# Kernel tuning notes

Measured on AMD Instinct MI355X. Metric: run time of the kernel, lower is better.

## Reference

```python
import jax, jax.numpy as jnp
import numpy as np

NUM_LAYERS = 2
D_MODEL = 64
D_INNER = 128   # expand * d_model
D_STATE = 128   # min(2*input_size, 256)
DT_RANK = 4     # ceil(d_model / 16)
D_CONV = 4
HIDDEN = 64


def _causal_dwconv(x, w, b):
    # x: [B, L, C], w: [C, K], b: [C]  -- causal depthwise conv (left pad K-1)
    K = w.shape[1]
    L = x.shape[1]
    xp = jnp.pad(x, ((0, 0), (K - 1, 0), (0, 0)))
    y = sum(xp[:, k:k + L, :] * w[:, k][None, None, :] for k in range(K))
    return y + b


def _selective_scan(u, delta, A, B, C, Dp):
    # u, delta: [b,L,d]; A: [d,n]; B, C: [b,L,n]; Dp: [d]
    dA = jnp.exp(jnp.einsum('bld,dn->lbdn', delta, A))          # [L,b,d,n]
    dBu = jnp.einsum('bld,bln,bld->lbdn', delta, B, u)           # [L,b,d,n]
    Ct = jnp.swapaxes(C, 0, 1)                                   # [L,b,n]

    def step(h, inp):
        dA_t, dBu_t, C_t = inp
        h = dA_t * h + dBu_t                                     # [b,d,n]
        y = jnp.einsum('bdn,bn->bd', h, C_t)
        return h, y

    h0 = jnp.zeros(dA.shape[1:], dA.dtype)
    _, ys = jax.lax.scan(step, h0, (dA, dBu, Ct))                # ys: [L,b,d]
    return jnp.swapaxes(ys, 0, 1) + u * Dp


def _mamba_layer(x, in_w, conv_w, conv_b, xproj_w, dt_w, dt_b, A_log, Dp, out_w):
    xz = x @ in_w.T                                              # [B,L,2*d_inner]
    xi, z = jnp.split(xz, 2, axis=-1)
    xi = jax.nn.silu(_causal_dwconv(xi, conv_w, conv_b))
    xdbl = xi @ xproj_w.T                                        # [B,L,dt_rank+2*d_state]
    delta = jax.nn.softplus(xdbl[..., :DT_RANK] @ dt_w.T + dt_b)
    Bm = xdbl[..., DT_RANK:DT_RANK + D_STATE]
    Cm = xdbl[..., DT_RANK + D_STATE:]
    A = -jnp.exp(A_log)
    y = _selective_scan(xi, delta, A, Bm, Cm, Dp)
    y = y * jax.nn.silu(z)
    return y @ out_w.T


def setup_inputs() -> dict:
    key = jax.random.key(0)
    ks = jax.random.split(key, 10)
    B, L = 4, 1024
    s = 0.05
    x = jax.random.normal(ks[0], (B, L, D_MODEL), dtype=jnp.float32)
    in_proj_w = jax.random.normal(ks[1], (NUM_LAYERS, 2 * D_INNER, D_MODEL)) * s
    conv_w = jax.random.normal(ks[2], (NUM_LAYERS, D_INNER, D_CONV)) * 0.2
    conv_b = jax.random.normal(ks[3], (NUM_LAYERS, D_INNER)) * 0.02
    x_proj_w = jax.random.normal(ks[4], (NUM_LAYERS, DT_RANK + 2 * D_STATE, D_INNER)) * s
    dt_w = jax.random.normal(ks[5], (NUM_LAYERS, D_INNER, DT_RANK)) * 0.1
    dt_b = jnp.full((NUM_LAYERS, D_INNER), -4.6, dtype=jnp.float32)  # softplus -> ~0.01
    # S4D-real init: A_log = log(1..d_state)
    A_log = jnp.log(jnp.broadcast_to(
        jnp.arange(1, D_STATE + 1, dtype=jnp.float32), (NUM_LAYERS, D_INNER, D_STATE)))
    D = jnp.ones((NUM_LAYERS, D_INNER), dtype=jnp.float32)
    out_proj_w = jax.random.normal(ks[6], (NUM_LAYERS, D_MODEL, D_INNER)) * s
    fc_w = jax.random.normal(ks[7], (HIDDEN, D_MODEL)) * s
    fc_b = jax.random.normal(ks[8], (HIDDEN,)) * 0.02
    return {"x": x, "in_proj_w": in_proj_w, "conv_w": conv_w, "conv_b": conv_b,
            "x_proj_w": x_proj_w, "dt_w": dt_w, "dt_b": dt_b, "A_log": A_log,
            "D": D, "out_proj_w": out_proj_w, "fc_w": fc_w, "fc_b": fc_b}


def reference(x, in_proj_w, conv_w, conv_b, x_proj_w, dt_w, dt_b, A_log, D, out_proj_w, fc_w, fc_b):
    h = x
    for l in range(NUM_LAYERS):
        h = _mamba_layer(h, in_proj_w[l], conv_w[l], conv_b[l], x_proj_w[l],
                         dt_w[l], dt_b[l], A_log[l], D[l], out_proj_w[l])
    return h @ fc_w.T + fc_b
```

## Files before the change

### kernel.cpp

```cpp
#include <hip/hip_runtime.h>
#include <hip/hip_bf16.h>

#define BB 4
#define LL 1024
#define DM 64
#define DI 128
#define DS 128
#define DTR 4
#define KC 4
#define RT 8
#define GRP 8
#define CS 64
#define NC 16
#define FQL 32
#define L2E 1.44269504f

#define XWT_OFF   0
#define INWT_OFF  65536
#define OWT_OFF   98304
#define CWT_OFF   114688
#define CB_OFF    115712
#define DTWT_OFF  115968
#define DTB_OFF   116992
#define XWDT_OFF  117248
#define WT_TOTAL  118272

__device__ __forceinline__ float silu_f(float x) { return x / (1.f + __expf(-x)); }
__device__ __forceinline__ float ex2(float x) { return __builtin_amdgcn_exp2f(x); }

__device__ __forceinline__ float ldf(const void* p, long i, unsigned bf) {
    return bf ? __bfloat162float(((const __hip_bfloat16*)p)[i]) : ((const float*)p)[i];
}

__device__ __forceinline__ void fma4(float4& acc, float s, const float4 w) {
    acc.x = fmaf(s, w.x, acc.x); acc.y = fmaf(s, w.y, acc.y);
    acc.z = fmaf(s, w.z, acc.z); acc.w = fmaf(s, w.w, acc.w);
}

__device__ __forceinline__ void probe_flags(const void* dtb, const void* fcw,
                                            unsigned& bfe, unsigned& bfw) {
    unsigned w = *(const unsigned*)dtb;
    bfe = (w == 0xC093C093u) ? 1u : 0u;
    const unsigned* p = (const unsigned*)fcw;
    int cnt = 0;
    for (int i = 0; i < 32; ++i) {
        unsigned m = p[i] & 0x7FFFu;
        if (m >= 0x3000u && m < 0x4200u) cnt++;
    }
    bfw = (cnt >= 28) ? 1u : 0u;
}

__global__ __launch_bounds__(256) void k_prep(
        const void* __restrict__ inw, const void* __restrict__ xw,
        const void* __restrict__ ow, const void* __restrict__ cw,
        const void* __restrict__ cb, const void* __restrict__ dtw,
        const void* __restrict__ dtb, const void* __restrict__ fcw,
        unsigned* __restrict__ flags, float* __restrict__ WT) {
    unsigned bfe, bfw;
    probe_flags(dtb, fcw, bfe, bfw);
    int bid = blockIdx.x, tid = threadIdx.x;
    if (bid < 28) {
        const void* src; long soff; int srcK; float* dst; int dstN; int n0, k0;
        if (bid < 16) {
            int l = bid >> 3, kt = (bid >> 2) & 1, nt = bid & 3;
            src = xw; srcK = 128; soff = (long)l * 260 * 128 + 4 * 128;
            n0 = nt * 64; k0 = kt * 64; dst = WT + XWT_OFF + l * 32768; dstN = 256;
        } else if (bid < 24) {
            int b2 = bid - 16, l = b2 >> 2, nt = b2 & 3;
            src = inw; srcK = 64; soff = (long)l * 256 * 64;
            n0 = nt * 64; k0 = 0; dst = WT + INWT_OFF + l * 16384; dstN = 256;
        } else {
            int b2 = bid - 24, l = b2 >> 1, kt = b2 & 1;
            src = ow; srcK = 128; soff = (long)l * 64 * 128;
            n0 = 0; k0 = kt * 64; dst = WT + OWT_OFF + l * 8192; dstN = 64;
        }
        __shared__ float tile[64 * 65];
        for (int i = tid; i < 4096; i += 256) {
            int ln = i >> 6, lk = i & 63;
            tile[ln * 65 + lk] = ldf(src, soff + (long)(n0 + ln) * srcK + k0 + lk, bfw);
        }
        __syncthreads();
        for (int i = tid; i < 4096; i += 256) {
            int lk = i >> 6, ln = i & 63;
            dst[(long)(k0 + lk) * dstN + n0 + ln] = tile[ln * 65 + lk];
        }
    } else {
        if (tid == 0) { flags[0] = bfe; flags[1] = bfw; flags[2] = bfe & bfw; }
        for (int j = tid; j < 1024; j += 256) {
            int l = j >> 9, t = (j >> 7) & 3, d = j & 127;
            WT[CWT_OFF + j] = ldf(cw, (long)l * 512 + d * 4 + t, bfw);
        }
        for (int j = tid; j < 256; j += 256) WT[CB_OFF + j] = ldf(cb, j, bfw);
        for (int j = tid; j < 1024; j += 256) {
            int l = j >> 9, r = (j >> 7) & 3, d = j & 127;
            WT[DTWT_OFF + j] = ldf(dtw, (long)l * 512 + d * 4 + r, bfw);
        }
        for (int j = tid; j < 256; j += 256) WT[DTB_OFF + j] = ldf(dtb, j, bfe);
        for (int j = tid; j < 1024; j += 256) {
            int l = j >> 9, rem = j & 511;
            WT[XWDT_OFF + j] = ldf(xw, (long)l * 260 * 128 + rem, bfw);
        }
    }
}

__global__ __launch_bounds__(256) void k_inx(
        const void* __restrict__ xin, int xin_probe,
        const float* __restrict__ inwT,
        const float* __restrict__ cwT, const float* __restrict__ cbF,
        const float* __restrict__ xwT, const float* __restrict__ xwdtF,
        const float* __restrict__ dtwT, const float* __restrict__ dtbF,
        const unsigned* __restrict__ flags,
        float* __restrict__ sz, float* __restrict__ xiw,
        float* __restrict__ dlt,
        float* __restrict__ Bm, float* __restrict__ Cm) {
    unsigned bfx = xin_probe ? flags[0] : 0u;
    int row0 = blockIdx.x * RT;
    int b = row0 >> 10, l0 = row0 & (LL - 1);
    int tid = threadIdx.x, lane = tid & 63, g = tid >> 6;
    __shared__ float xst[12 * DM];
    __shared__ float xc[12 * DI];
    __shared__ float act[RT * DI];
    __shared__ float dtp[RT * DTR];
    for (int i = tid; i < 12 * DM; i += 256) {
        int r = i >> 6;
        int l = l0 + r - (KC - 1);
        xst[i] = (l >= 0 && l < LL)
                 ? ldf(xin, ((long)b * LL + l) * DM + (i & 63), bfx) : 0.f;
    }
    __syncthreads();
    {
        const float4* wt4 = (const float4*)inwT;
        float4 acc[3];
        acc[0] = make_float4(0.f, 0.f, 0.f, 0.f);
        acc[1] = make_float4(0.f, 0.f, 0.f, 0.f);
        acc[2] = make_float4(0.f, 0.f, 0.f, 0.f);
#pragma unroll 4
        for (int k4 = 0; k4 < DM / 4; ++k4) {
            float4 w0 = wt4[(k4 * 4 + 0) * 64 + lane];
            float4 w1 = wt4[(k4 * 4 + 1) * 64 + lane];
            float4 w2 = wt4[(k4 * 4 + 2) * 64 + lane];
            float4 w3 = wt4[(k4 * 4 + 3) * 64 + lane];
#pragma unroll
            for (int r = 0; r < 3; ++r) {
                float4 av = *(const float4*)&xst[(g * 3 + r) * DM + k4 * 4];
                fma4(acc[r], av.x, w0); fma4(acc[r], av.y, w1);
                fma4(acc[r], av.z, w2); fma4(acc[r], av.w, w3);
            }
        }
        int n0 = lane * 4;
#pragma unroll
        for (int r = 0; r < 3; ++r) {
            int rr = g * 3 + r;
            if (n0 < DI) {
                *(float4*)&xc[rr * DI + n0] = acc[r];
            } else if (rr >= KC - 1 && rr < KC - 1 + RT) {
                float4 v;
                v.x = silu_f(acc[r].x); v.y = silu_f(acc[r].y);
                v.z = silu_f(acc[r].z); v.w = silu_f(acc[r].w);
                *(float4*)&sz[(size_t)(row0 + rr - (KC - 1)) * DI + (n0 - DI)] = v;
            }
        }
    }
    __syncthreads();
    for (int i = tid; i < RT * DI; i += 256) {
        int r = i >> 7, d = i & 127;
        float a = cbF[d];
#pragma unroll
        for (int t = 0; t < KC; ++t)
            a = fmaf(xc[(r + t) * DI + d], cwT[t * DI + d], a);
        float v = silu_f(a);
        act[i] = v;
        xiw[(size_t)(row0 + r) * DI + d] = v;
    }
    __syncthreads();
    {
        const float4* wt4 = (const float4*)xwT;
        float4 acc[2];
        acc[0] = make_float4(0.f, 0.f, 0.f, 0.f);
        acc[1] = make_float4(0.f, 0.f, 0.f, 0.f);
#pragma unroll 8
        for (int k4 = 0; k4 < DI / 4; ++k4) {
            float4 w0 = wt4[(k4 * 4 + 0) * 64 + lane];
            float4 w1 = wt4[(k4 * 4 + 1) * 64 + lane];
            float4 w2 = wt4[(k4 * 4 + 2) * 64 + lane];
            float4 w3 = wt4[(k4 * 4 + 3) * 64 + lane];
#pragma unroll
            for (int r = 0; r < 2; ++r) {
                float4 av = *(const float4*)&act[(g * 2 + r) * DI + k4 * 4];
                fma4(acc[r], av.x, w0); fma4(acc[r], av.y, w1);
                fma4(acc[r], av.z, w2); fma4(acc[r], av.w, w3);
            }
        }
        int n0 = lane * 4;
#pragma unroll
        for (int r = 0; r < 2; ++r) {
            int row = row0 + g * 2 + r;
            if (n0 < DS) *(float4*)&Bm[(size_t)row * DS + n0] = acc[r];
            else         *(float4*)&Cm[(size_t)row * DS + (n0 - DS)] = acc[r];
        }
    }
    if (tid < RT * DTR) {
        int r = tid >> 2, i = tid & 3;
        float a = 0.f;
#pragma unroll
        for (int k4 = 0; k4 < DI / 4; ++k4) {
            float4 av = *(const float4*)&act[r * DI + k4 * 4];
            float4 wv = *(const float4*)&xwdtF[i * DI + k4 * 4];
            a = fmaf(av.x, wv.x, a); a = fmaf(av.y, wv.y, a);
            a = fmaf(av.z, wv.z, a); a = fmaf(av.w, wv.w, a);
        }
        dtp[tid] = a;
    }
    __syncthreads();
    if (tid < DI) {
        float dw0 = dtwT[0 * DI + tid], dw1 = dtwT[1 * DI + tid];
        float dw2 = dtwT[2 * DI + tid], dw3 = dtwT[3 * DI + tid];
        float bv = dtbF[tid];
#pragma unroll
        for (int r = 0; r < RT; ++r) {
            float a = bv;
            a = fmaf(dtp[r * 4 + 0], dw0, a);
            a = fmaf(dtp[r * 4 + 1], dw1, a);
            a = fmaf(dtp[r * 4 + 2], dw2, a);
            a = fmaf(dtp[r * 4 + 3], dw3, a);
            dlt[(size_t)(row0 + r) * DI + tid] = (a > 20.f) ? a : log1pf(__expf(a));
        }
    }
}

__global__ __launch_bounds__(512) void k_scan1(
        const float* __restrict__ dlt, const float* __restrict__ xiw,
        const float* __restrict__ Bm, const float* __restrict__ Cm,
        const void* __restrict__ Alog, long aoff,
        const void* __restrict__ Dp, long doff,
        const unsigned* __restrict__ flags,
        float* __restrict__ hend, float* __restrict__ S,
        float* __restrict__ y) {
    __shared__ float Bsh[FQL][DS];
    __shared__ float Csh[FQL][DS];
    __shared__ float dsh[8][CS];
    __shared__ float dush[8][CS];
    __shared__ float ysh[CS][8];
    __shared__ float Wred[8 * 520];
    int gid = blockIdx.x;
    int dg = gid / (BB * NC);
    int bc = gid % (BB * NC);
    int b = bc / NC, c = bc % NC;
    int d0 = dg * 8;
    int tid = threadIdx.x, w = tid >> 6, t = tid & 63;
    int d = d0 + w, c0 = c * CS;
    unsigned bfe = flags[0];
    float A0 = -L2E * __expf(ldf(Alog, aoff + (long)d * DS + 2 * t, bfe));
    float A1 = -L2E * __expf(ldf(Alog, aoff + (long)d * DS + 2 * t + 1, bfe));
    {
        size_t src = ((size_t)b * LL + c0 + t) * DI + d0 + w;
        float dl = dlt[src], ul = xiw[src];
        dsh[w][t] = dl;
        dush[w][t] = dl * ul;
        ysh[t][w] = ul * ldf(Dp, doff + d0 + w, bfe);
    }
    float* Wl = Wred + w * 520;
    int rbase = (t >> 3) * 65 + (t & 7) * 8;
    float h0 = 0.f, h1v = 0.f, sumd = 0.f;
    for (int hh = 0; hh < 2; ++hh) {
        __syncthreads();
        for (int i = tid; i < FQL * 32; i += 512) {
            int r = i >> 5, c4 = (i & 31) * 4;
            size_t g = ((size_t)b * LL + c0 + hh * FQL + r) * DS + c4;
            *(float4*)&Bsh[r][c4] = *(const float4*)&Bm[g];
            *(float4*)&Csh[r][c4] = *(const float4*)&Cm[g];
        }
        __syncthreads();
        for (int li = 0; li < FQL; li += GRP) {
            int lg = hh * FQL + li;
            float dl[GRP], du[GRP], ea0[GRP], ea1[GRP], cv[GRP];
            float2 Bv[GRP], Cv[GRP];
#pragma unroll
            for (int s = 0; s < GRP; ++s) {
                dl[s] = dsh[w][lg + s];
                du[s] = dush[w][lg + s];
                Bv[s] = ((const float2*)Bsh[li + s])[t];
                Cv[s] = ((const float2*)Csh[li + s])[t];
            }
#pragma unroll
            for (int s = 0; s < GRP; ++s) {
                ea0[s] = ex2(dl[s] * A0);
                ea1[s] = ex2(dl[s] * A1);
                sumd += dl[s];
            }
#pragma unroll
            for (int s = 0; s < GRP; ++s) {
                h0  = fmaf(ea0[s], h0,  du[s] * Bv[s].x);
                h1v = fmaf(ea1[s], h1v, du[s] * Bv[s].y);
                cv[s] = fmaf(h0, Cv[s].x, h1v * Cv[s].y);
            }
#pragma unroll
            for (int s = 0; s < GRP; ++s) Wl[s * 65 + t] = cv[s];
            float pt = 0.f;
#pragma unroll
            for (int j = 0; j < 8; ++j) pt += Wl[rbase + j];
            pt += __shfl_xor(pt, 1, 64);
            pt += __shfl_xor(pt, 2, 64);
            pt += __shfl_xor(pt, 4, 64);
            if ((t & 7) == 0) ysh[lg + (t >> 3)][w] += pt;
        }
    }
    if (c < NC - 1) {
        size_t hbase = (((size_t)b * DI + d) * NC + c) * DS;
        ((float2*)(hend + hbase))[t] = make_float2(h0, h1v);
        if (t == 0) S[((size_t)b * DI + d) * NC + c] = sumd;
    }
    __syncthreads();
    for (int i = tid; i < CS * 8; i += 512) {
        int l = i >> 3, dd = i & 7;
        y[((size_t)b * LL + c0 + l) * DI + d0 + dd] = ysh[l][dd];
    }
}

__global__ __launch_bounds__(512) void k_scan2(
        const float* __restrict__ dlt, const float* __restrict__ Cm,
        const void* __restrict__ Alog, long aoff,
        const unsigned* __restrict__ flags,
        const float* __restrict__ hend, const float* __restrict__ S,
        float* __restrict__ y) {
    __shared__ float Csh[FQL][DS];
    __shared__ float cdsh[8][CS];
    __shared__ float ysh[CS][8];
    __shared__ float Wred[8 * 520];
    int gid = blockIdx.x;
    int dg = gid / (BB * (NC - 1));
    int bc = gid % (BB * (NC - 1));
    int b = bc / (NC - 1), c = bc % (NC - 1) + 1;
    int d0 = dg * 8;
    int tid = threadIdx.x, w = tid >> 6, t = tid & 63;
    int d = d0 + w, c0 = c * CS;
    unsigned bfe = flags[0];
    float A0 = -L2E * __expf(ldf(Alog, aoff + (long)d * DS + 2 * t, bfe));
    float A1 = -L2E * __expf(ldf(Alog, aoff + (long)d * DS + 2 * t + 1, bfe));
    {
        float a = dlt[((size_t)b * LL + c0 + t) * DI + d0 + w];
#pragma unroll
        for (int off = 1; off < 64; off <<= 1) {
            float nn = __shfl(a, t - off, 64);
            if (t >= off) a += nn;
        }
        cdsh[w][t] = a;
    }
    float hi0 = 0.f, hi1 = 0.f, ssum = 0.f;
    const float2* hep = (const float2*)(hend + (((size_t)b * DI + d) * NC) * DS);
    const float* Sp = S + ((size_t)b * DI + d) * NC;
    for (int cc = c - 1; cc >= 0; --cc) {
        float2 he = hep[(size_t)cc * (DS / 2) + t];
        hi0 = fmaf(ex2(A0 * ssum), he.x, hi0);
        hi1 = fmaf(ex2(A1 * ssum), he.y, hi1);
        ssum += Sp[cc];
    }
    float* Wl = Wred + w * 520;
    int rbase = (t >> 3) * 65 + (t & 7) * 8;
    for (int hh = 0; hh < 2; ++hh) {
        __syncthreads();
        for (int i = tid; i < FQL * 32; i += 512) {
            int r = i >> 5, c4 = (i & 31) * 4;
            *(float4*)&Csh[r][c4] =
                *(const float4*)&Cm[((size_t)b * LL + c0 + hh * FQL + r) * DS + c4];
        }
        __syncthreads();
        for (int li = 0; li < FQL; li += GRP) {
            int lg = hh * FQL + li;
            float cd[GRP], ea0[GRP], ea1[GRP], cv[GRP];
            float2 Cv[GRP];
#pragma unroll
            for (int s = 0; s < GRP; ++s) {
                cd[s] = cdsh[w][lg + s];
                Cv[s] = ((const float2*)Csh[li + s])[t];
            }
#pragma unroll
            for (int s = 0; s < GRP; ++s) {
                ea0[s] = ex2(cd[s] * A0);
                ea1[s] = ex2(cd[s] * A1);
            }
#pragma unroll
            for (int s = 0; s < GRP; ++s)
                cv[s] = fmaf(hi0 * ea0[s], Cv[s].x, hi1 * ea1[s] * Cv[s].y);
#pragma unroll
            for (int s = 0; s < GRP; ++s) Wl[s * 65 + t] = cv[s];
            float pt = 0.f;
#pragma unroll
            for (int j = 0; j < 8; ++j) pt += Wl[rbase + j];
            pt += __shfl_xor(pt, 1, 64);
            pt += __shfl_xor(pt, 2, 64);
            pt += __shfl_xor(pt, 4, 64);
            if ((t & 7) == 0) ysh[lg + (t >> 3)][w] = pt;
        }
    }
    __syncthreads();
    for (int i = tid; i < CS * 8; i += 512) {
        int l = i >> 3, dd = i & 7;
        size_t idx = ((size_t)b * LL + c0 + l) * DI + d0 + dd;
        y[idx] += ysh[l][dd];
    }
}

__global__ __launch_bounds__(256) void k_out(
        const float* __restrict__ y, const float* __restrict__ sz,
        const float* __restrict__ owT, float* __restrict__ hout) {
    int row0 = blockIdx.x * RT;
    int tid = threadIdx.x, n = tid & 63, g = tid >> 6;
    __shared__ float act[RT * DI];
    for (int i = tid; i < RT * DI; i += 256) {
        size_t idx = (size_t)(row0 + (i >> 7)) * DI + (i & 127);
        act[i] = y[idx] * sz[idx];
    }
    __syncthreads();
    float acc[2] = {0.f, 0.f};
#pragma unroll 8
    for (int k4 = 0; k4 < DI / 4; ++k4) {
        float w0 = owT[(k4 * 4 + 0) * DM + n];
        float w1 = owT[(k4 * 4 + 1) * DM + n];
        float w2 = owT[(k4 * 4 + 2) * DM + n];
        float w3 = owT[(k4 * 4 + 3) * DM + n];
#pragma unroll
        for (int r = 0; r < 2; ++r) {
            float4 av = *(const float4*)&act[(g * 2 + r) * DI + k4 * 4];
            acc[r] = fmaf(av.x, w0, acc[r]); acc[r] = fmaf(av.y, w1, acc[r]);
            acc[r] = fmaf(av.z, w2, acc[r]); acc[r] = fmaf(av.w, w3, acc[r]);
        }
    }
#pragma unroll
    for (int r = 0; r < 2; ++r)
        hout[(size_t)(row0 + g * 2 + r) * DM + n] = acc[r];
}

__global__ __launch_bounds__(256) void k_outfc(
        const float* __restrict__ y, const float* __restrict__ sz,
        const float* __restrict__ owT,
        const void* __restrict__ fw, const void* __restrict__ fb,
        const unsigned* __restrict__ flags, void* __restrict__ out) {
    unsigned bfw = flags[1], obf = flags[2];
    int row0 = blockIdx.x * RT;
    int tid = threadIdx.x, n = tid & 63, g = tid >> 6;
    __shared__ float act[RT * DI];
    __shared__ float wsh[DM * 65];
    __shared__ float hsh[RT * DM];
    for (int i = tid; i < RT * DI; i += 256) {
        size_t idx = (size_t)(row0 + (i >> 7)) * DI + (i & 127);
        act[i] = y[idx] * sz[idx];
    }
    for (int i = tid; i < DM * DM; i += 256) {
        int nn = i >> 6, k = i & 63;
        wsh[k * 65 + nn] = ldf(fw, i, bfw);
    }
    __syncthreads();
    float acc[2] = {0.f, 0.f};
#pragma unroll 8
    for (int k4 = 0; k4 < DI / 4; ++k4) {
        float w0 = owT[(k4 * 4 + 0) * DM + n];
        float w1 = owT[(k4 * 4 + 1) * DM + n];
        float w2 = owT[(k4 * 4 + 2) * DM + n];
        float w3 = owT[(k4 * 4 + 3) * DM + n];
#pragma unroll
        for (int r = 0; r < 2; ++r) {
            float4 av = *(const float4*)&act[(g * 2 + r) * DI + k4 * 4];
            acc[r] = fmaf(av.x, w0, acc[r]); acc[r] = fmaf(av.y, w1, acc[r]);
            acc[r] = fmaf(av.z, w2, acc[r]); acc[r] = fmaf(av.w, w3, acc[r]);
        }
    }
#pragma unroll
    for (int r = 0; r < 2; ++r) hsh[(g * 2 + r) * DM + n] = acc[r];
    __syncthreads();
    float bv = ldf(fb, n, bfw);
    float acc2[2] = {bv, bv};
#pragma unroll 8
    for (int k4 = 0; k4 < DM / 4; ++k4) {
        float w0 = wsh[(k4 * 4 + 0) * 65 + n];
        float w1 = wsh[(k4 * 4 + 1) * 65 + n];
        float w2 = wsh[(k4 * 4 + 2) * 65 + n];
        float w3 = wsh[(k4 * 4 + 3) * 65 + n];
#pragma unroll
        for (int r = 0; r < 2; ++r) {
            float4 av = *(const float4*)&hsh[(g * 2 + r) * DM + k4 * 4];
            acc2[r] = fmaf(av.x, w0, acc2[r]); acc2[r] = fmaf(av.y, w1, acc2[r]);
            acc2[r] = fmaf(av.z, w2, acc2[r]); acc2[r] = fmaf(av.w, w3, acc2[r]);
        }
    }
#pragma unroll
    for (int r = 0; r < 2; ++r) {
        size_t idx = (size_t)(row0 + g * 2 + r) * DM + n;
        if (obf) ((__hip_bfloat16*)out)[idx] = __float2bfloat16(acc2[r]);
        else     ((float*)out)[idx] = acc2[r];
    }
}

extern "C" void kernel_launch(void* const* d_in, const int* in_sizes, int n_in,
                              void* d_out, int out_size, void* d_ws, size_t ws_size,
                              hipStream_t stream) {
    const void* x    = d_in[0];
    const void* inw  = d_in[1];
    const void* cw   = d_in[2];
    const void* cb   = d_in[3];
    const void* xw   = d_in[4];
    const void* dtw  = d_in[5];
    const void* dtb  = d_in[6];
    const void* Alog = d_in[7];
    const void* Dp   = d_in[8];
    const void* ow   = d_in[9];
    const void* fcw  = d_in[10];
    const void* fcb  = d_in[11];

    const size_t NBL = (size_t)BB * LL;
    const int GB = (int)(NBL / RT);
    unsigned* flags = (unsigned*)d_ws;
    float* base = (float*)d_ws + 64;
    float* h1   = base;
    float* sz   = h1 + 262144;
    float* xiw  = sz + 524288;
    float* dlt  = xiw + 524288;
    float* Bmw  = dlt + 524288;
    float* Cmw  = Bmw + 524288;
    float* yw   = Cmw + 524288;
    float* hend = yw + 524288;
    float* S    = hend + 1048576;
    float* WT   = S + 8192;

    k_prep<<<29, 256, 0, stream>>>(inw, xw, ow, cw, cb, dtw, dtb, fcw, flags, WT);

    for (int l = 0; l < 2; ++l) {
        const void* xin = (l == 0) ? x : (const void*)h1;
        int xmode = (l == 0) ? 1 : 0;
        k_inx<<<GB, 256, 0, stream>>>(xin, xmode,
                                      WT + INWT_OFF + l * 16384,
                                      WT + CWT_OFF + l * 512, WT + CB_OFF + l * 128,
                                      WT + XWT_OFF + l * 32768, WT + XWDT_OFF + l * 512,
                                      WT + DTWT_OFF + l * 512, WT + DTB_OFF + l * 128,
                                      flags, sz, xiw, dlt, Bmw, Cmw);
        long ao = (long)l * DI * DS;
        long dof = (long)l * DI;
        k_scan1<<<16 * BB * NC, 512, 0, stream>>>(
            dlt, xiw, Bmw, Cmw, Alog, ao, Dp, dof, flags, hend, S, yw);
        k_scan2<<<16 * BB * (NC - 1), 512, 0, stream>>>(
            dlt, Cmw, Alog, ao, flags, hend, S, yw);
        if (l == 0) {
            k_out<<<GB, 256, 0, stream>>>(yw, sz, WT + OWT_OFF, h1);
        } else {
            k_outfc<<<GB, 256, 0, stream>>>(yw, sz, WT + OWT_OFF + 8192,
                                            fcw, fcb, flags, d_out);
        }
    }
}
```

Measured before the change: 291.7 us.

## Fuse two-pass chunked scan into one persistent kernel and fuse out/in projections

Merges the two chunked selective-scan kernels into one persistent kernel. Each chunk publishes its end state and delta sum with release flags, and later chunks spin-wait on those flags to fold in the carried state. It also fuses layer-0's output projection with layer-1's input projection, conv and x-projection, recomputing three halo rows per block. This cuts kernel launches and the y read-modify-write round trip, at the cost of cross-block spin waits that depend on all producer blocks being co-resident and on the ordering of work units.

```diff
diff --git a/kernel.cpp b/kernel.cpp
--- a/kernel.cpp
+++ b/kernel.cpp
@@ -13,6 +13,7 @@
 #define CS 64
 #define NC 16
 #define FQL 32
+#define NU 1024
 #define L2E 1.44269504f
 
 #define XWT_OFF   0
@@ -55,7 +56,8 @@
         const void* __restrict__ ow, const void* __restrict__ cw,
         const void* __restrict__ cb, const void* __restrict__ dtw,
         const void* __restrict__ dtb, const void* __restrict__ fcw,
-        unsigned* __restrict__ flags, float* __restrict__ WT) {
+        unsigned* __restrict__ flags, float* __restrict__ WT,
+        unsigned* __restrict__ FL) {
     unsigned bfe, bfw;
     probe_flags(dtb, fcw, bfe, bfw);
     int bid = blockIdx.x, tid = threadIdx.x;
@@ -86,6 +88,7 @@
         }
     } else {
         if (tid == 0) { flags[0] = bfe; flags[1] = bfw; flags[2] = bfe & bfw; }
+        for (int j = tid; j < 2 * NU; j += 256) FL[j] = 0u;
         for (int j = tid; j < 1024; j += 256) {
             int l = j >> 9, t = (j >> 7) & 3, d = j & 127;
             WT[CWT_OFF + j] = ldf(cw, (long)l * 512 + d * 4 + t, bfw);
@@ -228,207 +231,307 @@
     }
 }
 
-__global__ __launch_bounds__(512) void k_scan1(
+__global__ __launch_bounds__(512) void k_scanM(
         const float* __restrict__ dlt, const float* __restrict__ xiw,
         const float* __restrict__ Bm, const float* __restrict__ Cm,
         const void* __restrict__ Alog, long aoff,
         const void* __restrict__ Dp, long doff,
         const unsigned* __restrict__ flags,
-        float* __restrict__ hend, float* __restrict__ S,
+        unsigned long long* __restrict__ hend, float* __restrict__ S,
+        unsigned* __restrict__ FL, int lay,
         float* __restrict__ y) {
+    __shared__ float Csh[CS][DS];
     __shared__ float Bsh[FQL][DS];
-    __shared__ float Csh[FQL][DS];
     __shared__ float dsh[8][CS];
     __shared__ float dush[8][CS];
-    __shared__ float ysh[CS][8];
-    __shared__ float Wred[8 * 520];
-    int gid = blockIdx.x;
-    int dg = gid / (BB * NC);
-    int bc = gid % (BB * NC);
-    int b = bc / NC, c = bc % NC;
-    int d0 = dg * 8;
-    int tid = threadIdx.x, w = tid >> 6, t = tid & 63;
-    int d = d0 + w, c0 = c * CS;
-    unsigned bfe = flags[0];
-    float A0 = -L2E * __expf(ldf(Alog, aoff + (long)d * DS + 2 * t, bfe));
-    float A1 = -L2E * __expf(ldf(Alog, aoff + (long)d * DS + 2 * t + 1, bfe));
-    {
-        size_t src = ((size_t)b * LL + c0 + t) * DI + d0 + w;
-        float dl = dlt[src], ul = xiw[src];
-        dsh[w][t] = dl;
-        dush[w][t] = dl * ul;
-        ysh[t][w] = ul * ldf(Dp, doff + d0 + w, bfe);
-    }
-    float* Wl = Wred + w * 520;
-    int rbase = (t >> 3) * 65 + (t & 7) * 8;
-    float h0 = 0.f, h1v = 0.f, sumd = 0.f;
-    for (int hh = 0; hh < 2; ++hh) {
-        __syncthreads();
-        for (int i = tid; i < FQL * 32; i += 512) {
-            int r = i >> 5, c4 = (i & 31) * 4;
-            size_t g = ((size_t)b * LL + c0 + hh * FQL + r) * DS + c4;
-            *(float4*)&Bsh[r][c4] = *(const float4*)&Bm[g];
-            *(float4*)&Csh[r][c4] = *(const float4*)&Cm[g];
-        }
-        __syncthreads();
-        for (int li = 0; li < FQL; li += GRP) {
-            int lg = hh * FQL + li;
-            float dl[GRP], du[GRP], ea0[GRP], ea1[GRP], cv[GRP];
-            float2 Bv[GRP], Cv[GRP];
-#pragma unroll
-            for (int s = 0; s < GRP; ++s) {
-                dl[s] = dsh[w][lg + s];
-                du[s] = dush[w][lg + s];
-                Bv[s] = ((const float2*)Bsh[li + s])[t];
-                Cv[s] = ((const float2*)Csh[li + s])[t];
-            }
-#pragma unroll
-            for (int s = 0; s < GRP; ++s) {
-                ea0[s] = ex2(dl[s] * A0);
-                ea1[s] = ex2(dl[s] * A1);
-                sumd += dl[s];
-            }
-#pragma unroll
-            for (int s = 0; s < GRP; ++s) {
-                h0  = fmaf(ea0[s], h0,  du[s] * Bv[s].x);
-                h1v = fmaf(ea1[s], h1v, du[s] * Bv[s].y);
-                cv[s] = fmaf(h0, Cv[s].x, h1v * Cv[s].y);
-            }
-#pragma unroll
-            for (int s = 0; s < GRP; ++s) Wl[s * 65 + t] = cv[s];
-            float pt = 0.f;
-#pragma unroll
-            for (int j = 0; j < 8; ++j) pt += Wl[rbase + j];
-            pt += __shfl_xor(pt, 1, 64);
-            pt += __shfl_xor(pt, 2, 64);
-            pt += __shfl_xor(pt, 4, 64);
-            if ((t & 7) == 0) ysh[lg + (t >> 3)][w] += pt;
-        }
-    }
-    if (c < NC - 1) {
-        size_t hbase = (((size_t)b * DI + d) * NC + c) * DS;
-        ((float2*)(hend + hbase))[t] = make_float2(h0, h1v);
-        if (t == 0) S[((size_t)b * DI + d) * NC + c] = sumd;
-    }
-    __syncthreads();
-    for (int i = tid; i < CS * 8; i += 512) {
-        int l = i >> 3, dd = i & 7;
-        y[((size_t)b * LL + c0 + l) * DI + d0 + dd] = ysh[l][dd];
-    }
-}
-
-__global__ __launch_bounds__(512) void k_scan2(
-        const float* __restrict__ dlt, const float* __restrict__ Cm,
-        const void* __restrict__ Alog, long aoff,
-        const unsigned* __restrict__ flags,
-        const float* __restrict__ hend, const float* __restrict__ S,
-        float* __restrict__ y) {
-    __shared__ float Csh[FQL][DS];
     __shared__ float cdsh[8][CS];
     __shared__ float ysh[CS][8];
     __shared__ float Wred[8 * 520];
-    int gid = blockIdx.x;
-    int dg = gid / (BB * (NC - 1));
-    int bc = gid % (BB * (NC - 1));
-    int b = bc / (NC - 1), c = bc % (NC - 1) + 1;
-    int d0 = dg * 8;
     int tid = threadIdx.x, w = tid >> 6, t = tid & 63;
-    int d = d0 + w, c0 = c * CS;
     unsigned bfe = flags[0];
-    float A0 = -L2E * __expf(ldf(Alog, aoff + (long)d * DS + 2 * t, bfe));
-    float A1 = -L2E * __expf(ldf(Alog, aoff + (long)d * DS + 2 * t + 1, bfe));
-    {
-        float a = dlt[((size_t)b * LL + c0 + t) * DI + d0 + w];
-#pragma unroll
-        for (int off = 1; off < 64; off <<= 1) {
-            float nn = __shfl(a, t - off, 64);
-            if (t >= off) a += nn;
-        }
-        cdsh[w][t] = a;
-    }
-    float hi0 = 0.f, hi1 = 0.f, ssum = 0.f;
-    const float2* hep = (const float2*)(hend + (((size_t)b * DI + d) * NC) * DS);
-    const float* Sp = S + ((size_t)b * DI + d) * NC;
-    for (int cc = c - 1; cc >= 0; --cc) {
-        float2 he = hep[(size_t)cc * (DS / 2) + t];
-        hi0 = fmaf(ex2(A0 * ssum), he.x, hi0);
-        hi1 = fmaf(ex2(A1 * ssum), he.y, hi1);
-        ssum += Sp[cc];
-    }
     float* Wl = Wred + w * 520;
     int rbase = (t >> 3) * 65 + (t & 7) * 8;
-    for (int hh = 0; hh < 2; ++hh) {
+    for (int u = blockIdx.x; u < NU; u += gridDim.x) {
+        int dg = u >> 6, bc = u & 63, b = bc >> 4, c = bc & 15;
+        int d0 = dg * 8, d = d0 + w, c0 = c * CS;
+        float A0 = -L2E * __expf(ldf(Alog, aoff + (long)d * DS + 2 * t, bfe));
+        float A1 = -L2E * __expf(ldf(Alog, aoff + (long)d * DS + 2 * t + 1, bfe));
         __syncthreads();
-        for (int i = tid; i < FQL * 32; i += 512) {
+        {
+            size_t src = ((size_t)b * LL + c0 + t) * DI + d0 + w;
+            float dl = dlt[src], ul = xiw[src];
+            dsh[w][t] = dl;
+            dush[w][t] = dl * ul;
+            ysh[t][w] = ul * ldf(Dp, doff + d0 + w, bfe);
+            float a = dl;
+#pragma unroll
+            for (int off = 1; off < 64; off <<= 1) {
+                float nn = __shfl(a, t - off, 64);
+                if (t >= off) a += nn;
+            }
+            cdsh[w][t] = a;
+        }
+        for (int i = tid; i < CS * 32; i += 512) {
             int r = i >> 5, c4 = (i & 31) * 4;
             *(float4*)&Csh[r][c4] =
-                *(const float4*)&Cm[((size_t)b * LL + c0 + hh * FQL + r) * DS + c4];
+                *(const float4*)&Cm[((size_t)b * LL + c0 + r) * DS + c4];
+        }
+        float h0 = 0.f, h1v = 0.f;
+        for (int hh = 0; hh < 2; ++hh) {
+            if (hh) __syncthreads();
+            for (int i = tid; i < FQL * 32; i += 512) {
+                int r = i >> 5, c4 = (i & 31) * 4;
+                *(float4*)&Bsh[r][c4] =
+                    *(const float4*)&Bm[((size_t)b * LL + c0 + hh * FQL + r) * DS + c4];
+            }
+            __syncthreads();
+            for (int li = 0; li < FQL; li += GRP) {
+                int lg = hh * FQL + li;
+                float dl[GRP], du[GRP], ea0[GRP], ea1[GRP], cv[GRP];
+                float2 Bv[GRP], Cv[GRP];
+#pragma unroll
+                for (int s = 0; s < GRP; ++s) {
+                    dl[s] = dsh[w][lg + s];
+                    du[s] = dush[w][lg + s];
+                    Bv[s] = ((const float2*)Bsh[li + s])[t];
+                    Cv[s] = ((const float2*)Csh[lg + s])[t];
+                }
+#pragma unroll
+                for (int s = 0; s < GRP; ++s) {
+                    ea0[s] = ex2(dl[s] * A0);
+                    ea1[s] = ex2(dl[s] * A1);
+                }
+#pragma unroll
+                for (int s = 0; s < GRP; ++s) {
+                    h0  = fmaf(ea0[s], h0,  du[s] * Bv[s].x);
+                    h1v = fmaf(ea1[s], h1v, du[s] * Bv[s].y);
+                    cv[s] = fmaf(h0, Cv[s].x, h1v * Cv[s].y);
+                }
+#pragma unroll
+                for (int s = 0; s < GRP; ++s) Wl[s * 65 + t] = cv[s];
+                float pt = 0.f;
+#pragma unroll
+                for (int j = 0; j < 8; ++j) pt += Wl[rbase + j];
+                pt += __shfl_xor(pt, 1, 64);
+                pt += __shfl_xor(pt, 2, 64);
+                pt += __shfl_xor(pt, 4, 64);
+                if ((t & 7) == 0) ysh[lg + (t >> 3)][w] += pt;
+            }
+        }
+        if (c < NC - 1) {
+            size_t hb = (((size_t)b * DI + d) * NC + c) * (DS / 2) + t;
+            union { float2 f; unsigned long long q; } pk;
+            pk.f = make_float2(h0, h1v);
+            __hip_atomic_store(&hend[hb], pk.q, __ATOMIC_RELAXED,
+                               __HIP_MEMORY_SCOPE_AGENT);
+            if (t == 0)
+                __hip_atomic_store(&S[((size_t)b * DI + d) * NC + c], cdsh[w][CS - 1],
+                                   __ATOMIC_RELAXED, __HIP_MEMORY_SCOPE_AGENT);
+            __syncthreads();
+            if (tid == 0)
+                __hip_atomic_store(&FL[lay * NU + u], 1u, __ATOMIC_RELEASE,
+                                   __HIP_MEMORY_SCOPE_AGENT);
+        }
+        if (c > 0) {
+            if (tid == 0) {
+                int fb = lay * NU + (u - c);
+                for (int cc = 0; cc < c; ++cc)
+                    while (__hip_atomic_load(&FL[fb + cc], __ATOMIC_ACQUIRE,
+                                             __HIP_MEMORY_SCOPE_AGENT) == 0u)
+                        __builtin_amdgcn_s_sleep(8);
+            }
+            __syncthreads();
+            float hi0 = 0.f, hi1 = 0.f, ssum = 0.f;
+            for (int cc = c - 1; cc >= 0; --cc) {
+                size_t hb = (((size_t)b * DI + d) * NC + cc) * (DS / 2) + t;
+                union { float2 f; unsigned long long q; } pk;
+                pk.q = __hip_atomic_load(&hend[hb], __ATOMIC_RELAXED,
+                                         __HIP_MEMORY_SCOPE_AGENT);
+                float sv = __hip_atomic_load(&S[((size_t)b * DI + d) * NC + cc],
+                                             __ATOMIC_RELAXED, __HIP_MEMORY_SCOPE_AGENT);
+                hi0 = fmaf(ex2(A0 * ssum), pk.f.x, hi0);
+                hi1 = fmaf(ex2(A1 * ssum), pk.f.y, hi1);
+                ssum += sv;
+            }
+            for (int lg = 0; lg < CS; lg += GRP) {
+                float cd[GRP], ea0[GRP], ea1[GRP], cv[GRP];
+                float2 Cv[GRP];
+#pragma unroll
+                for (int s = 0; s < GRP; ++s) {
+                    cd[s] = cdsh[w][lg + s];
+                    Cv[s] = ((const float2*)Csh[lg + s])[t];
+                }
+#pragma unroll
+                for (int s = 0; s < GRP; ++s) {
+                    ea0[s] = ex2(cd[s] * A0);
+                    ea1[s] = ex2(cd[s] * A1);
+                }
+#pragma unroll
+                for (int s = 0; s < GRP; ++s)
+                    cv[s] = fmaf(hi0 * ea0[s], Cv[s].x, hi1 * ea1[s] * Cv[s].y);
+#pragma unroll
+                for (int s = 0; s < GRP; ++s) Wl[s * 65 + t] = cv[s];
+                float pt = 0.f;
+#pragma unroll
+                for (int j = 0; j < 8; ++j) pt += Wl[rbase + j];
+                pt += __shfl_xor(pt, 1, 64);
+                pt += __shfl_xor(pt, 2, 64);
+                pt += __shfl_xor(pt, 4, 64);
+                if ((t & 7) == 0) ysh[lg + (t >> 3)][w] += pt;
+            }
         }
         __syncthreads();
-        for (int li = 0; li < FQL; li += GRP) {
-            int lg = hh * FQL + li;
-            float cd[GRP], ea0[GRP], ea1[GRP], cv[GRP];
-            float2 Cv[GRP];
-#pragma unroll
-            for (int s = 0; s < GRP; ++s) {
-                cd[s] = cdsh[w][lg + s];
-                Cv[s] = ((const float2*)Csh[li + s])[t];
-            }
-#pragma unroll
-            for (int s = 0; s < GRP; ++s) {
-                ea0[s] = ex2(cd[s] * A0);
-                ea1[s] = ex2(cd[s] * A1);
-            }
-#pragma unroll
-            for (int s = 0; s < GRP; ++s)
-                cv[s] = fmaf(hi0 * ea0[s], Cv[s].x, hi1 * ea1[s] * Cv[s].y);
-#pragma unroll
-            for (int s = 0; s < GRP; ++s) Wl[s * 65 + t] = cv[s];
-            float pt = 0.f;
-#pragma unroll
-            for (int j = 0; j < 8; ++j) pt += Wl[rbase + j];
-            pt += __shfl_xor(pt, 1, 64);
-            pt += __shfl_xor(pt, 2, 64);
-            pt += __shfl_xor(pt, 4, 64);
-            if ((t & 7) == 0) ysh[lg + (t >> 3)][w] = pt;
-        }
-    }
-    __syncthreads();
-    for (int i = tid; i < CS * 8; i += 512) {
-        int l = i >> 3, dd = i & 7;
-        size_t idx = ((size_t)b * LL + c0 + l) * DI + d0 + dd;
-        y[idx] += ysh[l][dd];
-    }
-}
-
-__global__ __launch_bounds__(256) void k_out(
-        const float* __restrict__ y, const float* __restrict__ sz,
-        const float* __restrict__ owT, float* __restrict__ hout) {
+        for (int i = tid; i < CS * 8; i += 512) {
+            int l2 = i >> 3, dd = i & 7;
+            y[((size_t)b * LL + c0 + l2) * DI + d0 + dd] = ysh[l2][dd];
+        }
+    }
+}
+
+__global__ __launch_bounds__(256) void k_outinx(
+        const float* __restrict__ y, const float* __restrict__ sz0,
+        const float* __restrict__ owT,
+        const float* __restrict__ inwT,
+        const float* __restrict__ cwT, const float* __restrict__ cbF,
+        const float* __restrict__ xwT, const float* __restrict__ xwdtF,
+        const float* __restrict__ dtwT, const float* __restrict__ dtbF,
+        float* __restrict__ sz1, float* __restrict__ xiw,
+        float* __restrict__ dlt,
+        float* __restrict__ Bm, float* __restrict__ Cm) {
     int row0 = blockIdx.x * RT;
-    int tid = threadIdx.x, n = tid & 63, g = tid >> 6;
+    int b = row0 >> 10, l0 = row0 & (LL - 1);
+    int tid = threadIdx.x, lane = tid & 63, g = tid >> 6;
+    __shared__ float ya[12 * DI];
+    __shared__ float hsh[12 * DM];
+    __shared__ float xc[12 * DI];
     __shared__ float act[RT * DI];
+    __shared__ float dtp[RT * DTR];
+    for (int i = tid; i < 12 * DI; i += 256) {
+        int r = i >> 7;
+        int l = l0 + r - (KC - 1);
+        if (l >= 0 && l < LL) {
+            size_t idx = ((size_t)b * LL + l) * DI + (i & 127);
+            ya[i] = y[idx] * sz0[idx];
+        } else ya[i] = 0.f;
+    }
+    __syncthreads();
+    {
+        float acc[3] = {0.f, 0.f, 0.f};
+#pragma unroll 8
+        for (int k4 = 0; k4 < DI / 4; ++k4) {
+            float w0 = owT[(k4 * 4 + 0) * DM + lane];
+            float w1 = owT[(k4 * 4 + 1) * DM + lane];
+            float w2 = owT[(k4 * 4 + 2) * DM + lane];
+            float w3 = owT[(k4 * 4 + 3) * DM + lane];
+#pragma unroll
+            for (int r = 0; r < 3; ++r) {
+                float4 av = *(const float4*)&ya[(g * 3 + r) * DI + k4 * 4];
+                acc[r] = fmaf(av.x, w0, acc[r]); acc[r] = fmaf(av.y, w1, acc[r]);
+                acc[r] = fmaf(av.z, w2, acc[r]); acc[r] = fmaf(av.w, w3, acc[r]);
+            }
+        }
+#pragma unroll
+        for (int r = 0; r < 3; ++r) hsh[(g * 3 + r) * DM + lane] = acc[r];
+    }
+    __syncthreads();
+    {
+        const float4* wt4 = (const float4*)inwT;
+        float4 acc[3];
+        acc[0] = make_float4(0.f, 0.f, 0.f, 0.f);
+        acc[1] = make_float4(0.f, 0.f, 0.f, 0.f);
+        acc[2] = make_float4(0.f, 0.f, 0.f, 0.f);
+#pragma unroll 4
+        for (int k4 = 0; k4 < DM / 4; ++k4) {
+            float4 w0 = wt4[(k4 * 4 + 0) * 64 + lane];
+            float4 w1 = wt4[(k4 * 4 + 1) * 64 + lane];
+            float4 w2 = wt4[(k4 * 4 + 2) * 64 + lane];
+            float4 w3 = wt4[(k4 * 4 + 3) * 64 + lane];
+#pragma unroll
+            for (int r = 0; r < 3; ++r) {
+                float4 av = *(const float4*)&hsh[(g * 3 + r) * DM + k4 * 4];
+                fma4(acc[r], av.x, w0); fma4(acc[r], av.y, w1);
+                fma4(acc[r], av.z, w2); fma4(acc[r], av.w, w3);
+            }
+        }
+        int n0 = lane * 4;
+#pragma unroll
+        for (int r = 0; r < 3; ++r) {
+            int rr = g * 3 + r;
+            if (n0 < DI) {
+                *(float4*)&xc[rr * DI + n0] = acc[r];
+            } else if (rr >= KC - 1 && rr < KC - 1 + RT) {
+                float4 v;
+                v.x = silu_f(acc[r].x); v.y = silu_f(acc[r].y);
+                v.z = silu_f(acc[r].z); v.w = silu_f(acc[r].w);
+                *(float4*)&sz1[(size_t)(row0 + rr - (KC - 1)) * DI + (n0 - DI)] = v;
+            }
+        }
+    }
+    __syncthreads();
     for (int i = tid; i < RT * DI; i += 256) {
-        size_t idx = (size_t)(row0 + (i >> 7)) * DI + (i & 127);
-        act[i] = y[idx] * sz[idx];
-    }
-    __syncthreads();
-    float acc[2] = {0.f, 0.f};
+        int r = i >> 7, d = i & 127;
+        float a = cbF[d];
+#pragma unroll
+        for (int t = 0; t < KC; ++t)
+            a = fmaf(xc[(r + t) * DI + d], cwT[t * DI + d], a);
+        float v = silu_f(a);
+        act[i] = v;
+        xiw[(size_t)(row0 + r) * DI + d] = v;
+    }
+    __syncthreads();
+    {
+        const float4* wt4 = (const float4*)xwT;
+        float4 acc[2];
+        acc[0] = make_float4(0.f, 0.f, 0.f, 0.f);
+        acc[1] = make_float4(0.f, 0.f, 0.f, 0.f);
 #pragma unroll 8
-    for (int k4 = 0; k4 < DI / 4; ++k4) {
-        float w0 = owT[(k4 * 4 + 0) * DM + n];
-        float w1 = owT[(k4 * 4 + 1) * DM + n];
-        float w2 = owT[(k4 * 4 + 2) * DM + n];
-        float w3 = owT[(k4 * 4 + 3) * DM + n];
+        for (int k4 = 0; k4 < DI / 4; ++k4) {
+            float4 w0 = wt4[(k4 * 4 + 0) * 64 + lane];
+            float4 w1 = wt4[(k4 * 4 + 1) * 64 + lane];
+            float4 w2 = wt4[(k4 * 4 + 2) * 64 + lane];
+            float4 w3 = wt4[(k4 * 4 + 3) * 64 + lane];
+#pragma unroll
+            for (int r = 0; r < 2; ++r) {
+                float4 av = *(const float4*)&act[(g * 2 + r) * DI + k4 * 4];
+                fma4(acc[r], av.x, w0); fma4(acc[r], av.y, w1);
+                fma4(acc[r], av.z, w2); fma4(acc[r], av.w, w3);
+            }
+        }
+        int n0 = lane * 4;
 #pragma unroll
         for (int r = 0; r < 2; ++r) {
-            float4 av = *(const float4*)&act[(g * 2 + r) * DI + k4 * 4];
-            acc[r] = fmaf(av.x, w0, acc[r]); acc[r] = fmaf(av.y, w1, acc[r]);
-            acc[r] = fmaf(av.z, w2, acc[r]); acc[r] = fmaf(av.w, w3, acc[r]);
-        }
-    }
-#pragma unroll
-    for (int r = 0; r < 2; ++r)
-        hout[(size_t)(row0 + g * 2 + r) * DM + n] = acc[r];
+            int row = row0 + g * 2 + r;
+            if (n0 < DS) *(float4*)&Bm[(size_t)row * DS + n0] = acc[r];
+            else         *(float4*)&Cm[(size_t)row * DS + (n0 - DS)] = acc[r];
+        }
+    }
+    if (tid < RT * DTR) {
+        int r = tid >> 2, i = tid & 3;
+        float a = 0.f;
+#pragma unroll
+        for (int k4 = 0; k4 < DI / 4; ++k4) {
+            float4 av = *(const float4*)&act[r * DI + k4 * 4];
+            float4 wv = *(const float4*)&xwdtF[i * DI + k4 * 4];
+            a = fmaf(av.x, wv.x, a); a = fmaf(av.y, wv.y, a);
+            a = fmaf(av.z, wv.z, a); a = fmaf(av.w, wv.w, a);
+        }
+        dtp[tid] = a;
+    }
+    __syncthreads();
+    if (tid < DI) {
+        float dw0 = dtwT[0 * DI + tid], dw1 = dtwT[1 * DI + tid];
+        float dw2 = dtwT[2 * DI + tid], dw3 = dtwT[3 * DI + tid];
+        float bv = dtbF[tid];
+#pragma unroll
+        for (int r = 0; r < RT; ++r) {
+            float a = bv;
+            a = fmaf(dtp[r * 4 + 0], dw0, a);
+            a = fmaf(dtp[r * 4 + 1], dw1, a);
+            a = fmaf(dtp[r * 4 + 2], dw2, a);
+            a = fmaf(dtp[r * 4 + 3], dw3, a);
+            dlt[(size_t)(row0 + r) * DI + tid] = (a > 20.f) ? a : log1pf(__expf(a));
+        }
+    }
 }
 
 __global__ __launch_bounds__(256) void k_outfc(
@@ -507,43 +610,47 @@
     const void* fcw  = d_in[10];
     const void* fcb  = d_in[11];
 
-    const size_t NBL = (size_t)BB * LL;
-    const int GB = (int)(NBL / RT);
+    const int GB = (int)((size_t)BB * LL / RT);
     unsigned* flags = (unsigned*)d_ws;
     float* base = (float*)d_ws + 64;
-    float* h1   = base;
-    float* sz   = h1 + 262144;
-    float* xiw  = sz + 524288;
+    float* sz0  = base;
+    float* sz1  = sz0 + 524288;
+    float* xiw  = sz1 + 524288;
     float* dlt  = xiw + 524288;
     float* Bmw  = dlt + 524288;
     float* Cmw  = Bmw + 524288;
     float* yw   = Cmw + 524288;
-    float* hend = yw + 524288;
-    float* S    = hend + 1048576;
+    float* hendf = yw + 524288;
+    float* S    = hendf + 1048576;
     float* WT   = S + 8192;
-
-    k_prep<<<29, 256, 0, stream>>>(inw, xw, ow, cw, cb, dtw, dtb, fcw, flags, WT);
-
-    for (int l = 0; l < 2; ++l) {
-        const void* xin = (l == 0) ? x : (const void*)h1;
-        int xmode = (l == 0) ? 1 : 0;
-        k_inx<<<GB, 256, 0, stream>>>(xin, xmode,
-                                      WT + INWT_OFF + l * 16384,
-                                      WT + CWT_OFF + l * 512, WT + CB_OFF + l * 128,
-                                      WT + XWT_OFF + l * 32768, WT + XWDT_OFF + l * 512,
-                                      WT + DTWT_OFF + l * 512, WT + DTB_OFF + l * 128,
-                                      flags, sz, xiw, dlt, Bmw, Cmw);
-        long ao = (long)l * DI * DS;
-        long dof = (long)l * DI;
-        k_scan1<<<16 * BB * NC, 512, 0, stream>>>(
-            dlt, xiw, Bmw, Cmw, Alog, ao, Dp, dof, flags, hend, S, yw);
-        k_scan2<<<16 * BB * (NC - 1), 512, 0, stream>>>(
-            dlt, Cmw, Alog, ao, flags, hend, S, yw);
-        if (l == 0) {
-            k_out<<<GB, 256, 0, stream>>>(yw, sz, WT + OWT_OFF, h1);
-        } else {
-            k_outfc<<<GB, 256, 0, stream>>>(yw, sz, WT + OWT_OFF + 8192,
-                                            fcw, fcb, flags, d_out);
-        }
-    }
-}
+    unsigned* FL = (unsigned*)(WT + WT_TOTAL);
+    unsigned long long* hendq = (unsigned long long*)hendf;
+
+    int nb = 0;
+    hipOccupancyMaxActiveBlocksPerMultiprocessor(&nb, k_scanM, 512, 0);
+    if (nb < 1) nb = 1;
+    int gsz = nb * 256; if (gsz > NU) gsz = NU;
+
+    k_prep<<<29, 256, 0, stream>>>(inw, xw, ow, cw, cb, dtw, dtb, fcw,
+                                   flags, WT, FL);
+
+    k_inx<<<GB, 256, 0, stream>>>(x, 1,
+                                  WT + INWT_OFF,
+                                  WT + CWT_OFF, WT + CB_OFF,
+                                  WT + XWT_OFF, WT + XWDT_OFF,
+                                  WT + DTWT_OFF, WT + DTB_OFF,
+                                  flags, sz0, xiw, dlt, Bmw, Cmw);
+    k_scanM<<<gsz, 512, 0, stream>>>(dlt, xiw, Bmw, Cmw, Alog, 0L, Dp, 0L,
+                                     flags, hendq, S, FL, 0, yw);
+    k_outinx<<<GB, 256, 0, stream>>>(yw, sz0, WT + OWT_OFF,
+                                     WT + INWT_OFF + 16384,
+                                     WT + CWT_OFF + 512, WT + CB_OFF + 128,
+                                     WT + XWT_OFF + 32768, WT + XWDT_OFF + 512,
+                                     WT + DTWT_OFF + 512, WT + DTB_OFF + 128,
+                                     sz1, xiw, dlt, Bmw, Cmw);
+    k_scanM<<<gsz, 512, 0, stream>>>(dlt, xiw, Bmw, Cmw, Alog,
+                                     (long)DI * DS, Dp, (long)DI,
+                                     flags, hendq, S, FL, 1, yw);
+    k_outfc<<<GB, 256, 0, stream>>>(yw, sz1, WT + OWT_OFF + 8192,
+                                    fcw, fcb, flags, d_out);
+}
```

New measurement: 433.4 us. 48.6% more time.
